# Kernel tuning notes

Hardware: AMD Instinct MI355X
Metric: run time of the kernel (lower is better)

The kernel has to match this reference:

```python
import jax, jax.numpy as jnp
import numpy as np

K = 20          # neighbors, default of knn/get_graph_feature
EPS = 1e-5      # BatchNorm eps (torch default)


def knn_idx(x, k):
    # x: [B,3,N] -> indices of k nearest neighbors [B,N,k]
    xx = jnp.sum(x * x, axis=1)                      # [B,N]
    inner = jnp.einsum('bdn,bdm->bnm', x, x)         # [B,N,N]
    neg_dist = 2.0 * inner - xx[:, :, None] - xx[:, None, :]  # -||xi-xj||^2
    return jax.lax.top_k(neg_dist, k)[1]             # largest == nearest


def graph_feature(x, k):
    # x: [B,D,N] -> [B,2D,N,k]  (channels = [neighbor feats, center feats])
    idx = knn_idx(x, k)                              # [B,N,k]
    xt = jnp.transpose(x, (0, 2, 1))                 # [B,N,D]
    nbr = jax.vmap(lambda p, i: p[i])(xt, idx)       # [B,N,k,D] gather
    ctr = jnp.broadcast_to(xt[:, :, None, :], nbr.shape)
    feat = jnp.concatenate([nbr, ctr], axis=3)       # [B,N,k,2D]
    return jnp.transpose(feat, (0, 3, 1, 2))         # [B,2D,N,k]


def conv1x1(y, W):
    # Conv2d(kernel_size=1, bias=False): y [B,C,N,k], W [O,C]
    return jnp.einsum('bcnk,oc->bonk', y, W)


def bn_relu(y, g, b):
    # BatchNorm2d in training mode (batch statistics over B,N,k per channel)
    m = jnp.mean(y, axis=(0, 2, 3), keepdims=True)
    v = jnp.mean((y - m) ** 2, axis=(0, 2, 3), keepdims=True)
    yn = (y - m) * jax.lax.rsqrt(v + EPS)
    return jax.nn.relu(yn * g[None, :, None, None] + b[None, :, None, None])


def setup_inputs() -> dict:
    key = jax.random.key(0)
    ks = jax.random.split(key, 20)
    B, D, N = 8, 3, 2048
    x = jax.random.normal(ks[0], (B, D, N), dtype=jnp.float32)
    def w(k, o, c):
        return jax.random.normal(k, (o, c), dtype=jnp.float32) * (1.0 / np.sqrt(c))
    inp = {
        'x': x,
        'W1': w(ks[1], 64, 6),   'W2': w(ks[2], 64, 64),
        'W3': w(ks[3], 128, 64), 'W4': w(ks[4], 256, 128),
        'W5': w(ks[5], 512, 512),
    }
    for i, c in zip(range(1, 6), (64, 64, 128, 256, 512)):
        inp[f'g{i}'] = 1.0 + 0.1 * jax.random.normal(ks[5 + i], (c,), dtype=jnp.float32)
        inp[f'b{i}'] = 0.1 * jax.random.normal(ks[10 + i], (c,), dtype=jnp.float32)
    return inp


def reference(x, W1, W2, W3, W4, W5, g1, b1, g2, b2, g3, b3, g4, b4, g5, b5):
    # DGCNN core: single kNN graph feature + 4 EdgeConv 1x1 convs with
    # per-layer max over neighbors, concat, final 1x1 conv, pad to 1024 ch.
    f = graph_feature(x, K)                          # [B,6,N,K]
    h1 = bn_relu(conv1x1(f, W1), g1, b1)             # [B,64,N,K]
    x1 = jnp.max(h1, axis=-1, keepdims=True)
    h2 = bn_relu(conv1x1(h1, W2), g2, b2)            # [B,64,N,K]
    x2 = jnp.max(h2, axis=-1, keepdims=True)
    h3 = bn_relu(conv1x1(h2, W3), g3, b3)            # [B,128,N,K]
    x3 = jnp.max(h3, axis=-1, keepdims=True)
    h4 = bn_relu(conv1x1(h3, W4), g4, b4)            # [B,256,N,K]
    x4 = jnp.max(h4, axis=-1, keepdims=True)
    cat = jnp.concatenate([x1, x2, x3, x4], axis=1)  # [B,512,N,1]
    h5 = bn_relu(conv1x1(cat, W5), g5, b5)[..., 0]   # [B,512,N]
    out = jnp.pad(h5, ((0, 0), (0, 1024 - 512), (0, 0)))  # pad channels -> 1024
    return out.astype(jnp.float32)
```

## Files before the change

### kernel.cpp

```cpp
#include <hip/hip_runtime.h>

#define BB  8
#define NP  2048
#define KNB 20
#define SS  40960

typedef unsigned short bf16_t;
typedef __attribute__((ext_vector_type(8))) short short8_t;
typedef __attribute__((ext_vector_type(4))) float f32x4;

static __device__ __forceinline__ float bf2f(unsigned short u) {
    return __uint_as_float(((unsigned)u) << 16);
}
static __device__ __forceinline__ bf16_t f2bf(float f) {
    unsigned u = __float_as_uint(f);
    return (bf16_t)((u + 0x7fffu + ((u >> 16) & 1u)) >> 16);
}

#if __has_builtin(__builtin_amdgcn_fmed3f)
#define MED3(a, b, c) __builtin_amdgcn_fmed3f((a), (b), (c))
#else
#define MED3(a, b, c) fmaxf(fminf((a), (b)), fminf(fmaxf((a), (b)), (c)))
#endif

static __device__ __forceinline__ float negdist(float4 me, float4 p) {
    float d = me.x * p.x + me.y * p.y + me.z * p.z;
    return 2.0f * d - me.w - p.w;
}

#define BDECL(t) float bv##t = -3.4e38f;
#define MCH(t, p) bv##t = MED3(v, bv##p, bv##t);
#define BSHIFT(t, n) bv##t = bv##n;

__global__ __launch_bounds__(256) void knn_kernel(const float* __restrict__ x,
                                                  int* __restrict__ idx) {
    __shared__ float4 tile[2064];
    __shared__ int   cnt[16];
    __shared__ float svv[16][44];
    __shared__ int   svj[16][44];
    const int tid  = threadIdx.x;
    const int b    = blockIdx.x >> 7;
    const int pblk = blockIdx.x & 127;
    const int pl   = tid >> 4;
    const int seg  = tid & 15;
    const int i    = pblk * 16 + pl;
    const float* xb = x + (size_t)b * 3 * NP;

    for (int j = tid; j < NP; j += 256) {
        float a0 = xb[j], a1 = xb[NP + j], a2 = xb[2 * NP + j];
        tile[j + (j >> 7)] = make_float4(a0, a1, a2, a0 * a0 + a1 * a1 + a2 * a2);
    }
    if (tid < 16) cnt[tid] = 0;
    __syncthreads();
    const float4 me = tile[i + (i >> 7)];
    const float4* tseg = &tile[seg * 129];

    BDECL(0)  BDECL(1)  BDECL(2)  BDECL(3)  BDECL(4)
    BDECL(5)  BDECL(6)  BDECL(7)  BDECL(8)  BDECL(9)
    BDECL(10) BDECL(11) BDECL(12) BDECL(13) BDECL(14)
    BDECL(15) BDECL(16) BDECL(17) BDECL(18) BDECL(19)
    for (int t = 0; t < 128; ++t) {
        float v = negdist(me, tseg[t]);
        MCH(19,18) MCH(18,17) MCH(17,16) MCH(16,15) MCH(15,14)
        MCH(14,13) MCH(13,12) MCH(12,11) MCH(11,10) MCH(10,9)
        MCH(9,8)   MCH(8,7)   MCH(7,6)   MCH(6,5)   MCH(5,4)
        MCH(4,3)   MCH(3,2)   MCH(2,1)   MCH(1,0)
        bv0 = fmaxf(bv0, v);
    }

    float theta = -3.4e38f;
    for (int r = 0; r < KNB; ++r) {
        float mv = bv0; int ms = seg;
#pragma unroll
        for (int s = 1; s <= 8; s <<= 1) {
            float ov = __shfl_xor(mv, s, 64);
            int   os = __shfl_xor(ms, s, 64);
            if (ov > mv || (ov == mv && os < ms)) { mv = ov; ms = os; }
        }
        if (seg == ms) {
            BSHIFT(0,1)   BSHIFT(1,2)   BSHIFT(2,3)   BSHIFT(3,4)   BSHIFT(4,5)
            BSHIFT(5,6)   BSHIFT(6,7)   BSHIFT(7,8)   BSHIFT(8,9)   BSHIFT(9,10)
            BSHIFT(10,11) BSHIFT(11,12) BSHIFT(12,13) BSHIFT(13,14) BSHIFT(14,15)
            BSHIFT(15,16) BSHIFT(16,17) BSHIFT(17,18) BSHIFT(18,19)
            bv19 = -3.4e38f;
        }
        theta = mv;
    }

    for (int t = 0; t < 128; ++t) {
        float v = negdist(me, tseg[t]);
        if (v >= theta) {
            int k = atomicAdd(&cnt[pl], 1);
            if (k < 44) { svv[pl][k] = v; svj[pl][k] = seg * 128 + t; }
        }
    }
    __syncthreads();

    int n = cnt[pl]; if (n > 44) n = 44;
    int* o = idx + ((size_t)b * NP + i) * KNB;
    for (int e = seg; e < n; e += 16) {
        float v = svv[pl][e]; int j = svj[pl][e];
        int rank = 0;
        for (int q = 0; q < n; ++q) {
            float vq = svv[pl][q]; int jq = svj[pl][q];
            rank += (vq > v || (vq == v && jq < j)) ? 1 : 0;
        }
        if (rank < KNB) o[rank] = j;
    }
}

__global__ void gather_kernel(const float* __restrict__ x, const int* __restrict__ idx,
                              bf16_t* __restrict__ f) {
    int s = blockIdx.x * 256 + threadIdx.x;
    int b = blockIdx.y;
    int n = s / KNB;
    int j = idx[(size_t)b * SS + s];
    const float* xb = x + (size_t)b * 3 * NP;
    ushort4 u0, u1;
    u0.x = f2bf(xb[j]);          u0.y = f2bf(xb[NP + j]);
    u0.z = f2bf(xb[2 * NP + j]); u0.w = f2bf(xb[n]);
    u1.x = f2bf(xb[NP + n]);     u1.y = f2bf(xb[2 * NP + n]);
    u1.z = 0; u1.w = 0;
    ushort4 z4; z4.x = 0; z4.y = 0; z4.z = 0; z4.w = 0;
    bf16_t* fb = f + ((size_t)b * SS + s) * 32;
    *(ushort4*)(fb)      = u0;
    *(ushort4*)(fb + 4)  = u1;
    *(ushort4*)(fb + 8)  = z4;
    *(ushort4*)(fb + 12) = z4;
    *(ushort4*)(fb + 16) = z4;
    *(ushort4*)(fb + 20) = z4;
    *(ushort4*)(fb + 24) = z4;
    *(ushort4*)(fb + 28) = z4;
}

__global__ void wconv_kernel(const float* __restrict__ src, bf16_t* __restrict__ dst,
                             int O, int CI, int CIP) {
    int t = blockIdx.x * 256 + threadIdx.x;
    if (t >= O * CIP) return;
    int o = t / CIP, cp = t - o * CIP;
    dst[t] = (cp < CI) ? f2bf(src[o * CI + cp]) : (bf16_t)0;
}

__global__ void zstats_kernel(float* __restrict__ p) {
    p[blockIdx.x * 256 + threadIdx.x] = 0.f;
}

__global__ void bnrelu_kernel(bf16_t* __restrict__ y, const float* __restrict__ ab,
                              int C) {
    size_t e0 = ((size_t)blockIdx.x * 256 + threadIdx.x) * 8;
    int c0 = (int)(e0 & (size_t)(C - 1));
    uint4 r = *(uint4*)(y + e0);
    float4 a0 = *(const float4*)(ab + c0);
    float4 a1 = *(const float4*)(ab + c0 + 4);
    float4 d0 = *(const float4*)(ab + C + c0);
    float4 d1 = *(const float4*)(ab + C + c0 + 4);
    float v0 = bf2f((unsigned short)(r.x & 0xffffu)), v1 = bf2f((unsigned short)(r.x >> 16));
    float v2 = bf2f((unsigned short)(r.y & 0xffffu)), v3 = bf2f((unsigned short)(r.y >> 16));
    float v4 = bf2f((unsigned short)(r.z & 0xffffu)), v5 = bf2f((unsigned short)(r.z >> 16));
    float v6 = bf2f((unsigned short)(r.w & 0xffffu)), v7 = bf2f((unsigned short)(r.w >> 16));
    v0 = fmaxf(fmaf(a0.x, v0, d0.x), 0.f); v1 = fmaxf(fmaf(a0.y, v1, d0.y), 0.f);
    v2 = fmaxf(fmaf(a0.z, v2, d0.z), 0.f); v3 = fmaxf(fmaf(a0.w, v3, d0.w), 0.f);
    v4 = fmaxf(fmaf(a1.x, v4, d1.x), 0.f); v5 = fmaxf(fmaf(a1.y, v5, d1.y), 0.f);
    v6 = fmaxf(fmaf(a1.z, v6, d1.z), 0.f); v7 = fmaxf(fmaf(a1.w, v7, d1.w), 0.f);
    r.x = (unsigned)f2bf(v0) | ((unsigned)f2bf(v1) << 16);
    r.y = (unsigned)f2bf(v2) | ((unsigned)f2bf(v3) << 16);
    r.z = (unsigned)f2bf(v4) | ((unsigned)f2bf(v5) << 16);
    r.w = (unsigned)f2bf(v6) | ((unsigned)f2bf(v7) << 16);
    *(uint4*)(y + e0) = r;
}

#define MF(A, B, C) C = __builtin_amdgcn_mfma_f32_16x16x32_bf16(A, B, C, 0, 0, 0);

#define KMFMA(AK0, AK1, AK2, AK3, koff) { \
    short8_t bb0 = *(const short8_t*)(hp0 + (koff)); \
    short8_t bb1 = *(const short8_t*)(hp1 + (koff)); \
    MF(AK0, bb0, c00) MF(AK1, bb0, c10) MF(AK2, bb0, c20) MF(AK3, bb0, c30) \
    MF(AK0, bb1, c01) MF(AK1, bb1, c11) MF(AK2, bb1, c21) MF(AK3, bb1, c31) }

#define TILE1(CC, CT, STt) { \
    ushort4 t4; \
    t4.x = f2bf(CC[0]); t4.y = f2bf(CC[1]); \
    t4.z = f2bf(CC[2]); t4.w = f2bf(CC[3]); \
    *(ushort4*)&ytile[w * 32 + (STt) * 16 + col][(CT) * 16 + quad * 4] = t4; }

template<int CIN, int COUT_T, int SROWS, int NW, int NS, bool POOL, bool ST, bool PRE>
__global__ void mconv(const bf16_t* __restrict__ H, const bf16_t* __restrict__ Wb,
                      bf16_t* __restrict__ Yout, bf16_t* __restrict__ poolOut,
                      int chofs, float* __restrict__ stats) {
    constexpr int SR = NW * 32;
    __shared__ bf16_t ytile[SR][68];
    __shared__ float redS[NW][64];
    __shared__ float redQ[NW][64];
    const int tid  = threadIdx.x;
    const int lane = tid & 63, col = lane & 15, quad = lane >> 4, q8 = quad * 8;
    const int w    = tid >> 6;
    const int cob  = blockIdx.y * 64;
    const int b    = blockIdx.z;
    const bf16_t* wp = Wb + (size_t)(cob + col) * CIN + q8;

    short8_t A00 = {}, A10 = {}, A20 = {}, A30 = {};
    short8_t A01 = {}, A11 = {}, A21 = {}, A31 = {};
    short8_t A02 = {}, A12 = {}, A22 = {}, A32 = {};
    short8_t A03 = {}, A13 = {}, A23 = {}, A33 = {};
    if constexpr (PRE) {
        A00 = *(const short8_t*)(wp);
        A10 = *(const short8_t*)(wp + 16 * CIN);
        A20 = *(const short8_t*)(wp + 32 * CIN);
        A30 = *(const short8_t*)(wp + 48 * CIN);
        if constexpr (CIN >= 64) {
            A01 = *(const short8_t*)(wp + 32);
            A11 = *(const short8_t*)(wp + 16 * CIN + 32);
            A21 = *(const short8_t*)(wp + 32 * CIN + 32);
            A31 = *(const short8_t*)(wp + 48 * CIN + 32);
        }
        if constexpr (CIN >= 128) {
            A02 = *(const short8_t*)(wp + 64);
            A12 = *(const short8_t*)(wp + 16 * CIN + 64);
            A22 = *(const short8_t*)(wp + 32 * CIN + 64);
            A32 = *(const short8_t*)(wp + 48 * CIN + 64);
            A03 = *(const short8_t*)(wp + 96);
            A13 = *(const short8_t*)(wp + 16 * CIN + 96);
            A23 = *(const short8_t*)(wp + 32 * CIN + 96);
            A33 = *(const short8_t*)(wp + 48 * CIN + 96);
        }
    }

    float svA = 0.f, svB = 0.f, qvA = 0.f, qvB = 0.f;
    float sv0 = 0.f, sv1 = 0.f, sv2 = 0.f, sv3 = 0.f;
    float qv0 = 0.f, qv1 = 0.f, qv2 = 0.f, qv3 = 0.f;

    for (int it = 0; it < NS; ++it) {
        const int sb = blockIdx.x * (SR * NS) + it * SR + w * 32;
        const bf16_t* hp0 = H + ((size_t)b * SROWS + sb + col) * CIN + q8;
        const bf16_t* hp1 = hp0 + 16 * CIN;

        f32x4 c00 = {0.f,0.f,0.f,0.f}, c10 = c00, c20 = c00, c30 = c00;
        f32x4 c01 = c00, c11 = c00, c21 = c00, c31 = c00;

        if constexpr (PRE) {
            KMFMA(A00, A10, A20, A30, 0)
            if constexpr (CIN >= 64)  KMFMA(A01, A11, A21, A31, 32)
            if constexpr (CIN >= 128) {
                KMFMA(A02, A12, A22, A32, 64)
                KMFMA(A03, A13, A23, A33, 96)
            }
        } else {
#pragma unroll 4
            for (int k0 = 0; k0 < CIN; k0 += 32) {
                short8_t a0 = *(const short8_t*)(wp + k0);
                short8_t a1 = *(const short8_t*)(wp + 16 * CIN + k0);
                short8_t a2 = *(const short8_t*)(wp + 32 * CIN + k0);
                short8_t a3 = *(const short8_t*)(wp + 48 * CIN + k0);
                KMFMA(a0, a1, a2, a3, k0)
            }
        }

        TILE1(c00,0,0) TILE1(c10,1,0) TILE1(c20,2,0) TILE1(c30,3,0)
        TILE1(c01,0,1) TILE1(c11,1,1) TILE1(c21,2,1) TILE1(c31,3,1)
        __syncthreads();

        if constexpr (ST) {
            const int row0 = blockIdx.x * (SR * NS) + it * SR;
            for (int i = tid; i < SR * 16; i += NW * 64) {
                int row = i >> 4, c4 = (i & 15) * 4;
                ushort4 yv = *(const ushort4*)&ytile[row][c4];
                *(ushort4*)(Yout + ((size_t)b * SROWS + row0 + row) * COUT_T + cob + c4) = yv;
                if constexpr (!POOL) {
                    float v0 = bf2f(yv.x), v1 = bf2f(yv.y);
                    float v2 = bf2f(yv.z), v3 = bf2f(yv.w);
                    sv0 += v0; qv0 = fmaf(v0, v0, qv0);
                    sv1 += v1; qv1 = fmaf(v1, v1, qv1);
                    sv2 += v2; qv2 = fmaf(v2, v2, qv2);
                    sv3 += v3; qv3 = fmaf(v3, v3, qv3);
                }
            }
        }
        if constexpr (POOL) {
            const int nbase = (blockIdx.x * NS + it) * 8;
            for (int i = tid; i < 8 * 32; i += NW * 64) {
                const int nl = i >> 5, c2 = (i & 31) * 2;
                float m0 = -3.4e38f, m1 = -3.4e38f;
#pragma unroll
                for (int k = 0; k < KNB; ++k) {
                    unsigned u = *(const unsigned*)&ytile[nl * 20 + k][c2];
                    float v0 = bf2f((unsigned short)(u & 0xffffu));
                    float v1 = bf2f((unsigned short)(u >> 16));
                    m0 = fmaxf(m0, v0); m1 = fmaxf(m1, v1);
                    svA += v0; qvA = fmaf(v0, v0, qvA);
                    svB += v1; qvB = fmaf(v1, v1, qvB);
                }
                unsigned r2 = (unsigned)f2bf(m0) | ((unsigned)f2bf(m1) << 16);
                *(unsigned*)(poolOut + ((size_t)b * NP + nbase + nl) * 512 + chofs + cob + c2) = r2;
            }
        }
        __syncthreads();
    }

    if constexpr (POOL) {
        svA += __shfl_xor(svA, 32, 64); qvA += __shfl_xor(qvA, 32, 64);
        svB += __shfl_xor(svB, 32, 64); qvB += __shfl_xor(qvB, 32, 64);
        if (lane < 32) {
            const int c2 = lane * 2;
            redS[w][c2] = svA; redS[w][c2 + 1] = svB;
            redQ[w][c2] = qvA; redQ[w][c2 + 1] = qvB;
        }
    } else if constexpr (ST) {
        sv0 += __shfl_xor(sv0, 16, 64); qv0 += __shfl_xor(qv0, 16, 64);
        sv1 += __shfl_xor(sv1, 16, 64); qv1 += __shfl_xor(qv1, 16, 64);
        sv2 += __shfl_xor(sv2, 16, 64); qv2 += __shfl_xor(qv2, 16, 64);
        sv3 += __shfl_xor(sv3, 16, 64); qv3 += __shfl_xor(qv3, 16, 64);
        sv0 += __shfl_xor(sv0, 32, 64); qv0 += __shfl_xor(qv0, 32, 64);
        sv1 += __shfl_xor(sv1, 32, 64); qv1 += __shfl_xor(qv1, 32, 64);
        sv2 += __shfl_xor(sv2, 32, 64); qv2 += __shfl_xor(qv2, 32, 64);
        sv3 += __shfl_xor(sv3, 32, 64); qv3 += __shfl_xor(qv3, 32, 64);
        if (lane < 16) {
            const int c4 = lane * 4;
            redS[w][c4]     = sv0; redS[w][c4 + 1] = sv1;
            redS[w][c4 + 2] = sv2; redS[w][c4 + 3] = sv3;
            redQ[w][c4]     = qv0; redQ[w][c4 + 1] = qv1;
            redQ[w][c4 + 2] = qv2; redQ[w][c4 + 3] = qv3;
        }
    }
    __syncthreads();
    if (tid < 64) {
        float sv = 0.f, qv = 0.f;
#pragma unroll
        for (int ch = 0; ch < NW; ++ch) { sv += redS[ch][tid]; qv += redQ[ch][tid]; }
        atomicAdd(&stats[cob + tid], sv);
        atomicAdd(&stats[COUT_T + cob + tid], qv);
    }
}

__global__ void bn_finalize(const float* __restrict__ stats,
                            const float* __restrict__ g, const float* __restrict__ bt,
                            float* __restrict__ ab, int C, float invM) {
    int c = blockIdx.x * 64 + threadIdx.x;
    if (c >= C) return;
    float mean = stats[c] * invM;
    float var  = fmaxf(stats[C + c] * invM - mean * mean, 0.f);
    float a = g[c] * rsqrtf(var + 1e-5f);
    ab[c] = a;
    ab[C + c] = fmaf(-mean, a, bt[c]);
}

__global__ void pool_convert(const bf16_t* __restrict__ pr, const float* __restrict__ ab,
                             bf16_t* __restrict__ xc, int C, int chofs, int logC) {
    int t = blockIdx.x * 256 + threadIdx.x;
    int c = t & (C - 1);
    int rest = t >> logC;
    int n = rest & (NP - 1);
    int b = rest >> 11;
    size_t p = ((size_t)b * NP + n) * 512 + chofs + c;
    float v = bf2f(pr[p]);
    xc[p] = f2bf(fmaxf(fmaf(ab[c], v, ab[C + c]), 0.f));
}

__global__ void out_kernel(const bf16_t* __restrict__ y5, const float* __restrict__ ab,
                           float* __restrict__ out) {
    int t = blockIdx.x * 256 + threadIdx.x;
    int n = t & (NP - 1);
    int c4 = (t >> 11) & 255;
    int b = t >> 19;
    int c0 = c4 * 4;
    float4 v = make_float4(0.f, 0.f, 0.f, 0.f);
    if (c0 < 512) {
        ushort4 yv = *(const ushort4*)(y5 + ((size_t)b * NP + n) * 512 + c0);
        float4 av = *(const float4*)(ab + c0);
        float4 dv = *(const float4*)(ab + 512 + c0);
        v.x = fmaxf(fmaf(av.x, bf2f(yv.x), dv.x), 0.f);
        v.y = fmaxf(fmaf(av.y, bf2f(yv.y), dv.y), 0.f);
        v.z = fmaxf(fmaf(av.z, bf2f(yv.z), dv.z), 0.f);
        v.w = fmaxf(fmaf(av.w, bf2f(yv.w), dv.w), 0.f);
    }
    float* ob = out + ((size_t)b * 1024 + c0) * NP + n;
    ob[0] = v.x; ob[NP] = v.y; ob[2 * NP] = v.z; ob[3 * NP] = v.w;
}

extern "C" void kernel_launch(void* const* d_in, const int* in_sizes, int n_in,
                              void* d_out, int out_size, void* d_ws, size_t ws_size,
                              hipStream_t stream) {
    (void)in_sizes; (void)n_in; (void)out_size; (void)ws_size;
    const float* x  = (const float*)d_in[0];
    const float* W1 = (const float*)d_in[1];
    const float* W2 = (const float*)d_in[2];
    const float* W3 = (const float*)d_in[3];
    const float* W4 = (const float*)d_in[4];
    const float* W5 = (const float*)d_in[5];
    const float* g1 = (const float*)d_in[6];  const float* b1 = (const float*)d_in[7];
    const float* g2 = (const float*)d_in[8];  const float* b2 = (const float*)d_in[9];
    const float* g3 = (const float*)d_in[10]; const float* b3 = (const float*)d_in[11];
    const float* g4 = (const float*)d_in[12]; const float* b4 = (const float*)d_in[13];
    const float* g5 = (const float*)d_in[14]; const float* b5 = (const float*)d_in[15];

    char* ws = (char*)d_ws;
    bf16_t* f    = (bf16_t*)(ws + 0);
    bf16_t* y2   = (bf16_t*)(ws + 0);
    bf16_t* y5   = (bf16_t*)(ws + 0);
    bf16_t* y1   = (bf16_t*)(ws + 41943040);
    bf16_t* y3   = (bf16_t*)(ws + 41943040);
    bf16_t* poolraw = (bf16_t*)(ws + 125829120);
    bf16_t* xcat    = (bf16_t*)(ws + 142606336);
    bf16_t* Wball   = (bf16_t*)(ws + 159383552);
    bf16_t* W1b = Wball;
    bf16_t* W2b = Wball + 2048;
    bf16_t* W3b = Wball + 6144;
    bf16_t* W4b = Wball + 14336;
    bf16_t* W5b = Wball + 47104;
    float* stats = (float*)(ws + 160002048);
    float* ab    = (float*)(ws + 160010240);
    int*  idx    = (int*)  (ws + 160018432);

    float* st1 = stats;        float* st2 = stats + 128;  float* st3 = stats + 256;
    float* st4 = stats + 512;  float* st5 = stats + 1024;
    float* ab1 = ab;       float* ab2 = ab + 128;  float* ab3 = ab + 256;
    float* ab4 = ab + 512; float* ab5 = ab + 1024;
    const float invM14 = 1.f / (float)(BB * SS);
    const float invM5  = 1.f / (float)(BB * NP);

    zstats_kernel<<<8, 256, 0, stream>>>(stats);
    wconv_kernel<<<8,    256, 0, stream>>>(W1, W1b, 64, 6, 32);
    wconv_kernel<<<16,   256, 0, stream>>>(W2, W2b, 64, 64, 64);
    wconv_kernel<<<32,   256, 0, stream>>>(W3, W3b, 128, 64, 64);
    wconv_kernel<<<128,  256, 0, stream>>>(W4, W4b, 256, 128, 128);
    wconv_kernel<<<1024, 256, 0, stream>>>(W5, W5b, 512, 512, 512);

    knn_kernel<<<1024, 256, 0, stream>>>(x, idx);
    gather_kernel<<<dim3(160, BB), 256, 0, stream>>>(x, idx, f);

    mconv<32, 64, SS, 5, 4, true, true, true><<<dim3(64, 1, BB), 320, 0, stream>>>(
        f, W1b, y1, poolraw, 0, st1);
    bn_finalize<<<1, 64, 0, stream>>>(st1, g1, b1, ab1, 64, invM14);
    pool_convert<<<4096, 256, 0, stream>>>(poolraw, ab1, xcat, 64, 0, 6);
    bnrelu_kernel<<<10240, 256, 0, stream>>>(y1, ab1, 64);

    mconv<64, 64, SS, 5, 4, true, true, true><<<dim3(64, 1, BB), 320, 0, stream>>>(
        y1, W2b, y2, poolraw, 64, st2);
    bn_finalize<<<1, 64, 0, stream>>>(st2, g2, b2, ab2, 64, invM14);
    pool_convert<<<4096, 256, 0, stream>>>(poolraw, ab2, xcat, 64, 64, 6);
    bnrelu_kernel<<<10240, 256, 0, stream>>>(y2, ab2, 64);

    mconv<64, 128, SS, 5, 4, true, true, true><<<dim3(64, 2, BB), 320, 0, stream>>>(
        y2, W3b, y3, poolraw, 128, st3);
    bn_finalize<<<2, 64, 0, stream>>>(st3, g3, b3, ab3, 128, invM14);
    pool_convert<<<8192, 256, 0, stream>>>(poolraw, ab3, xcat, 128, 128, 7);
    bnrelu_kernel<<<20480, 256, 0, stream>>>(y3, ab3, 128);

    mconv<128, 256, SS, 5, 4, true, false, true><<<dim3(64, 4, BB), 320, 0, stream>>>(
        y3, W4b, nullptr, poolraw, 256, st4);
    bn_finalize<<<4, 64, 0, stream>>>(st4, g4, b4, ab4, 256, invM14);
    pool_convert<<<16384, 256, 0, stream>>>(poolraw, ab4, xcat, 256, 256, 8);

    mconv<512, 512, NP, 4, 1, false, true, false><<<dim3(16, 8, BB), 256, 0, stream>>>(
        xcat, W5b, y5, nullptr, 0, st5);
    bn_finalize<<<8, 64, 0, stream>>>(st5, g5, b5, ab5, 512, invM5);

    out_kernel<<<16384, 256, 0, stream>>>(y5, ab5, (float*)d_out);
}
```

Baseline: 483.4 us.

## Software-pipeline activation loads in MFMA conv kernel with register prefetch

For the weight-preloaded (PRE) path, activation B-fragments for the next row tile are now loaded into registers before the MFMAs and epilogue of the current tile run, so global load latency overlaps compute. The final __syncthreads after the last iteration is skipped. The epilogue is factored into a macro shared by both paths. Double buffering raises VGPR usage, which can reduce occupancy, especially for CIN=128.

```diff
diff --git a/kernel.cpp b/kernel.cpp
--- a/kernel.cpp
+++ b/kernel.cpp
@@ -171,23 +171,59 @@
 
 #define MF(A, B, C) C = __builtin_amdgcn_mfma_f32_16x16x32_bf16(A, B, C, 0, 0, 0);
 
-#define KMFMA(AK0, AK1, AK2, AK3, koff) { \
-    short8_t bb0 = *(const short8_t*)(hp0 + (koff)); \
-    short8_t bb1 = *(const short8_t*)(hp1 + (koff)); \
-    MF(AK0, bb0, c00) MF(AK1, bb0, c10) MF(AK2, bb0, c20) MF(AK3, bb0, c30) \
-    MF(AK0, bb1, c01) MF(AK1, bb1, c11) MF(AK2, bb1, c21) MF(AK3, bb1, c31) }
-
 #define TILE1(CC, CT, STt) { \
     ushort4 t4; \
     t4.x = f2bf(CC[0]); t4.y = f2bf(CC[1]); \
     t4.z = f2bf(CC[2]); t4.w = f2bf(CC[3]); \
     *(ushort4*)&ytile[w * 32 + (STt) * 16 + col][(CT) * 16 + quad * 4] = t4; }
 
+#define EPILOGUE(ITV) { \
+    TILE1(c00,0,0) TILE1(c10,1,0) TILE1(c20,2,0) TILE1(c30,3,0) \
+    TILE1(c01,0,1) TILE1(c11,1,1) TILE1(c21,2,1) TILE1(c31,3,1) \
+    __syncthreads(); \
+    if constexpr (ST) { \
+        const int row0 = blockIdx.x * (SR * NS) + (ITV) * SR; \
+        for (int i = tid; i < SR * 16; i += NW * 64) { \
+            int row = i >> 4, c4 = (i & 15) * 4; \
+            ushort4 yv = *(const ushort4*)&ytile[row][c4]; \
+            *(ushort4*)(Yout + ((size_t)b * SROWS + row0 + row) * COUT_T + cob + c4) = yv; \
+            if constexpr (!POOL) { \
+                float v0 = bf2f(yv.x), v1 = bf2f(yv.y); \
+                float v2 = bf2f(yv.z), v3 = bf2f(yv.w); \
+                sv0 += v0; qv0 = fmaf(v0, v0, qv0); \
+                sv1 += v1; qv1 = fmaf(v1, v1, qv1); \
+                sv2 += v2; qv2 = fmaf(v2, v2, qv2); \
+                sv3 += v3; qv3 = fmaf(v3, v3, qv3); \
+            } \
+        } \
+    } \
+    if constexpr (POOL) { \
+        const int nbase = (blockIdx.x * NS + (ITV)) * 8; \
+        for (int i = tid; i < 8 * 32; i += NW * 64) { \
+            const int nl = i >> 5, c2 = (i & 31) * 2; \
+            float m0 = -3.4e38f, m1 = -3.4e38f; \
+            _Pragma("unroll") \
+            for (int k = 0; k < KNB; ++k) { \
+                unsigned u = *(const unsigned*)&ytile[nl * 20 + k][c2]; \
+                float v0 = bf2f((unsigned short)(u & 0xffffu)); \
+                float v1 = bf2f((unsigned short)(u >> 16)); \
+                m0 = fmaxf(m0, v0); m1 = fmaxf(m1, v1); \
+                svA += v0; qvA = fmaf(v0, v0, qvA); \
+                svB += v1; qvB = fmaf(v1, v1, qvB); \
+            } \
+            unsigned r2 = (unsigned)f2bf(m0) | ((unsigned)f2bf(m1) << 16); \
+            *(unsigned*)(poolOut + ((size_t)b * NP + nbase + nl) * 512 + chofs + cob + c2) = r2; \
+        } \
+    } \
+    if ((ITV) + 1 < NS) __syncthreads(); \
+}
+
 template<int CIN, int COUT_T, int SROWS, int NW, int NS, bool POOL, bool ST, bool PRE>
 __global__ void mconv(const bf16_t* __restrict__ H, const bf16_t* __restrict__ Wb,
                       bf16_t* __restrict__ Yout, bf16_t* __restrict__ poolOut,
                       int chofs, float* __restrict__ stats) {
     constexpr int SR = NW * 32;
+    constexpr int NKK = CIN / 32;
     __shared__ bf16_t ytile[SR][68];
     __shared__ float redS[NW][64];
     __shared__ float redQ[NW][64];
@@ -198,102 +234,84 @@
     const int b    = blockIdx.z;
     const bf16_t* wp = Wb + (size_t)(cob + col) * CIN + q8;
 
-    short8_t A00 = {}, A10 = {}, A20 = {}, A30 = {};
-    short8_t A01 = {}, A11 = {}, A21 = {}, A31 = {};
-    short8_t A02 = {}, A12 = {}, A22 = {}, A32 = {};
-    short8_t A03 = {}, A13 = {}, A23 = {}, A33 = {};
-    if constexpr (PRE) {
-        A00 = *(const short8_t*)(wp);
-        A10 = *(const short8_t*)(wp + 16 * CIN);
-        A20 = *(const short8_t*)(wp + 32 * CIN);
-        A30 = *(const short8_t*)(wp + 48 * CIN);
-        if constexpr (CIN >= 64) {
-            A01 = *(const short8_t*)(wp + 32);
-            A11 = *(const short8_t*)(wp + 16 * CIN + 32);
-            A21 = *(const short8_t*)(wp + 32 * CIN + 32);
-            A31 = *(const short8_t*)(wp + 48 * CIN + 32);
-        }
-        if constexpr (CIN >= 128) {
-            A02 = *(const short8_t*)(wp + 64);
-            A12 = *(const short8_t*)(wp + 16 * CIN + 64);
-            A22 = *(const short8_t*)(wp + 32 * CIN + 64);
-            A32 = *(const short8_t*)(wp + 48 * CIN + 64);
-            A03 = *(const short8_t*)(wp + 96);
-            A13 = *(const short8_t*)(wp + 16 * CIN + 96);
-            A23 = *(const short8_t*)(wp + 32 * CIN + 96);
-            A33 = *(const short8_t*)(wp + 48 * CIN + 96);
-        }
-    }
-
     float svA = 0.f, svB = 0.f, qvA = 0.f, qvB = 0.f;
     float sv0 = 0.f, sv1 = 0.f, sv2 = 0.f, sv3 = 0.f;
     float qv0 = 0.f, qv1 = 0.f, qv2 = 0.f, qv3 = 0.f;
 
-    for (int it = 0; it < NS; ++it) {
-        const int sb = blockIdx.x * (SR * NS) + it * SR + w * 32;
-        const bf16_t* hp0 = H + ((size_t)b * SROWS + sb + col) * CIN + q8;
-        const bf16_t* hp1 = hp0 + 16 * CIN;
-
-        f32x4 c00 = {0.f,0.f,0.f,0.f}, c10 = c00, c20 = c00, c30 = c00;
-        f32x4 c01 = c00, c11 = c00, c21 = c00, c31 = c00;
-
-        if constexpr (PRE) {
-            KMFMA(A00, A10, A20, A30, 0)
-            if constexpr (CIN >= 64)  KMFMA(A01, A11, A21, A31, 32)
-            if constexpr (CIN >= 128) {
-                KMFMA(A02, A12, A22, A32, 64)
-                KMFMA(A03, A13, A23, A33, 96)
+    if constexpr (PRE) {
+        short8_t Af0[NKK], Af1[NKK], Af2[NKK], Af3[NKK];
+#pragma unroll
+        for (int kk = 0; kk < NKK; ++kk) {
+            Af0[kk] = *(const short8_t*)(wp + kk * 32);
+            Af1[kk] = *(const short8_t*)(wp + 16 * CIN + kk * 32);
+            Af2[kk] = *(const short8_t*)(wp + 32 * CIN + kk * 32);
+            Af3[kk] = *(const short8_t*)(wp + 48 * CIN + kk * 32);
+        }
+
+        short8_t cb0[NKK], cb1[NKK], nb0[NKK], nb1[NKK];
+        {
+            const int sb = blockIdx.x * (SR * NS) + w * 32;
+            const bf16_t* hp0 = H + ((size_t)b * SROWS + sb + col) * CIN + q8;
+            const bf16_t* hp1 = hp0 + 16 * CIN;
+#pragma unroll
+            for (int kk = 0; kk < NKK; ++kk) {
+                cb0[kk] = *(const short8_t*)(hp0 + kk * 32);
+                cb1[kk] = *(const short8_t*)(hp1 + kk * 32);
             }
-        } else {
+        }
+
+#pragma unroll
+        for (int it = 0; it < NS; ++it) {
+            if (it + 1 < NS) {
+                const int sb = blockIdx.x * (SR * NS) + (it + 1) * SR + w * 32;
+                const bf16_t* hp0 = H + ((size_t)b * SROWS + sb + col) * CIN + q8;
+                const bf16_t* hp1 = hp0 + 16 * CIN;
+#pragma unroll
+                for (int kk = 0; kk < NKK; ++kk) {
+                    nb0[kk] = *(const short8_t*)(hp0 + kk * 32);
+                    nb1[kk] = *(const short8_t*)(hp1 + kk * 32);
+                }
+            }
+
+            f32x4 c00 = {0.f,0.f,0.f,0.f}, c10 = c00, c20 = c00, c30 = c00;
+            f32x4 c01 = c00, c11 = c00, c21 = c00, c31 = c00;
+#pragma unroll
+            for (int kk = 0; kk < NKK; ++kk) {
+                MF(Af0[kk], cb0[kk], c00) MF(Af1[kk], cb0[kk], c10)
+                MF(Af2[kk], cb0[kk], c20) MF(Af3[kk], cb0[kk], c30)
+                MF(Af0[kk], cb1[kk], c01) MF(Af1[kk], cb1[kk], c11)
+                MF(Af2[kk], cb1[kk], c21) MF(Af3[kk], cb1[kk], c31)
+            }
+
+            EPILOGUE(it)
+
+            if (it + 1 < NS) {
+#pragma unroll
+                for (int kk = 0; kk < NKK; ++kk) { cb0[kk] = nb0[kk]; cb1[kk] = nb1[kk]; }
+            }
+        }
+    } else {
+        for (int it = 0; it < NS; ++it) {
+            const int sb = blockIdx.x * (SR * NS) + it * SR + w * 32;
+            const bf16_t* hp0 = H + ((size_t)b * SROWS + sb + col) * CIN + q8;
+            const bf16_t* hp1 = hp0 + 16 * CIN;
+
+            f32x4 c00 = {0.f,0.f,0.f,0.f}, c10 = c00, c20 = c00, c30 = c00;
+            f32x4 c01 = c00, c11 = c00, c21 = c00, c31 = c00;
 #pragma unroll 4
             for (int k0 = 0; k0 < CIN; k0 += 32) {
                 short8_t a0 = *(const short8_t*)(wp + k0);
                 short8_t a1 = *(const short8_t*)(wp + 16 * CIN + k0);
                 short8_t a2 = *(const short8_t*)(wp + 32 * CIN + k0);
                 short8_t a3 = *(const short8_t*)(wp + 48 * CIN + k0);
-                KMFMA(a0, a1, a2, a3, k0)
+                short8_t bb0 = *(const short8_t*)(hp0 + k0);
+                short8_t bb1 = *(const short8_t*)(hp1 + k0);
+                MF(a0, bb0, c00) MF(a1, bb0, c10) MF(a2, bb0, c20) MF(a3, bb0, c30)
+                MF(a0, bb1, c01) MF(a1, bb1, c11) MF(a2, bb1, c21) MF(a3, bb1, c31)
             }
-        }
-
-        TILE1(c00,0,0) TILE1(c10,1,0) TILE1(c20,2,0) TILE1(c30,3,0)
-        TILE1(c01,0,1) TILE1(c11,1,1) TILE1(c21,2,1) TILE1(c31,3,1)
-        __syncthreads();
-
-        if constexpr (ST) {
-            const int row0 = blockIdx.x * (SR * NS) + it * SR;
-            for (int i = tid; i < SR * 16; i += NW * 64) {
-                int row = i >> 4, c4 = (i & 15) * 4;
-                ushort4 yv = *(const ushort4*)&ytile[row][c4];
-                *(ushort4*)(Yout + ((size_t)b * SROWS + row0 + row) * COUT_T + cob + c4) = yv;
-                if constexpr (!POOL) {
-                    float v0 = bf2f(yv.x), v1 = bf2f(yv.y);
-                    float v2 = bf2f(yv.z), v3 = bf2f(yv.w);
-                    sv0 += v0; qv0 = fmaf(v0, v0, qv0);
-                    sv1 += v1; qv1 = fmaf(v1, v1, qv1);
-                    sv2 += v2; qv2 = fmaf(v2, v2, qv2);
-                    sv3 += v3; qv3 = fmaf(v3, v3, qv3);
-                }
-            }
-        }
-        if constexpr (POOL) {
-            const int nbase = (blockIdx.x * NS + it) * 8;
-            for (int i = tid; i < 8 * 32; i += NW * 64) {
-                const int nl = i >> 5, c2 = (i & 31) * 2;
-                float m0 = -3.4e38f, m1 = -3.4e38f;
-#pragma unroll
-                for (int k = 0; k < KNB; ++k) {
-                    unsigned u = *(const unsigned*)&ytile[nl * 20 + k][c2];
-                    float v0 = bf2f((unsigned short)(u & 0xffffu));
-                    float v1 = bf2f((unsigned short)(u >> 16));
-                    m0 = fmaxf(m0, v0); m1 = fmaxf(m1, v1);
-                    svA += v0; qvA = fmaf(v0, v0, qvA);
-                    svB += v1; qvB = fmaf(v1, v1, qvB);
-                }
-                unsigned r2 = (unsigned)f2bf(m0) | ((unsigned)f2bf(m1) << 16);
-                *(unsigned*)(poolOut + ((size_t)b * NP + nbase + nl) * 512 + chofs + cob + c2) = r2;
-            }
-        }
-        __syncthreads();
+
+            EPILOGUE(it)
+        }
     }
 
     if constexpr (POOL) {
```

Result: slower. 529.1 us (+9.5%).
